# Performance work log

Hardware: AMD Instinct MI355X
Metric: run time of the kernel (lower is better)

## Reference

```python
import jax, jax.numpy as jnp
import numpy as np

EMBED_DIM = 1024
NUM_HEADS = 16
HEAD_DIM = EMBED_DIM // NUM_HEADS
BSZ = 4
SEQ = 1500


def setup_inputs() -> dict:
    key = jax.random.key(0)
    ks = jax.random.split(key, 8)
    s = 0.02
    return {
        "hidden_states": jax.random.normal(ks[0], (BSZ, SEQ, EMBED_DIM), jnp.float32),
        "Wq": jax.random.normal(ks[1], (EMBED_DIM, EMBED_DIM), jnp.float32) * s,
        "bq": jax.random.normal(ks[2], (EMBED_DIM,), jnp.float32) * s,
        "Wk": jax.random.normal(ks[3], (EMBED_DIM, EMBED_DIM), jnp.float32) * s,
        "Wv": jax.random.normal(ks[4], (EMBED_DIM, EMBED_DIM), jnp.float32) * s,
        "bv": jax.random.normal(ks[5], (EMBED_DIM,), jnp.float32) * s,
        "Wo": jax.random.normal(ks[6], (EMBED_DIM, EMBED_DIM), jnp.float32) * s,
        "bo": jax.random.normal(ks[7], (EMBED_DIM,), jnp.float32) * s,
    }


def reference(hidden_states, Wq, bq, Wk, Wv, bv, Wo, bo):
    b, t, e = hidden_states.shape
    h, d = NUM_HEADS, HEAD_DIM
    scaling = d ** -0.5

    def shape(x):  # [b, t, e] -> [b, h, t, d]
        return x.reshape(b, t, h, d).transpose(0, 2, 1, 3)

    # q_proj (with bias) then scale applied to the full projected output,
    # matching the original (scale multiplies q_proj output incl. bias).
    q = shape((hidden_states @ Wq.T + bq) * scaling)
    k = shape(hidden_states @ Wk.T)            # k_proj has no bias in Whisper
    v = shape(hidden_states @ Wv.T + bv)

    # naive materialized attention scores: [b, h, t, t]
    attn_weights = jnp.einsum("bhqd,bhkd->bhqk", q, k)
    attn_probs = jax.nn.softmax(attn_weights, axis=-1)
    attn_output = jnp.einsum("bhqk,bhkd->bhqd", attn_probs, v)

    # [b, h, t, d] -> [b, t, e]
    attn_output = attn_output.transpose(0, 2, 1, 3).reshape(b, t, e)
    return attn_output @ Wo.T + bo
```

## Files before the change

### kernel.cpp

```cpp
#include <hip/hip_runtime.h>
#include <math.h>

#define E 1024
#define NH 16
#define HD 64
#define BSZ_ 4
#define SEQ_ 1500
#define M_ (BSZ_ * SEQ_)
#define SZE ((size_t)M_ * (size_t)E)
#define QSC (0.125f * 1.44269504f)

#define QA_OFF  0u
#define XB_OFF  6144000u
#define WB_OFF  12288000u
#define WOB_OFF 15433728u
#define WS_NEED_BYTES ((size_t)(16482304u) * 2u)

typedef __attribute__((ext_vector_type(8))) short short8v;
typedef __attribute__((ext_vector_type(4))) float f32x4;
typedef __attribute__((ext_vector_type(16))) float f32x16;
typedef __attribute__((ext_vector_type(4))) unsigned short ushort4v;

__device__ __forceinline__ unsigned short f2bf(float f) {
    union { float f; unsigned int i; } c; c.f = f;
    return (unsigned short)((c.i + 0x7FFFu + ((c.i >> 16) & 1u)) >> 16);
}
__device__ __forceinline__ unsigned int cvt_pk_bf16(float a, float b) {
    unsigned int r;
    asm("v_cvt_pk_bf16_f32 %0, %1, %2" : "=v"(r) : "v"(a), "v"(b));
    return r;
}
__device__ __forceinline__ void perml32(unsigned int &a, unsigned int &b) {
    asm("v_permlane32_swap_b32 %0, %1" : "+v"(a), "+v"(b));
}

__device__ __forceinline__ int swz(int row, int col) {
    return (row << 6) + ((((col >> 3) ^ row) & 7) << 3) + (col & 7);
}
__device__ __forceinline__ int swzf(int r, int d) {
    int row = r >> 1;
    int cs = ((r & 1) << 3) | (d >> 3);
    return row * 128 + ((cs ^ (row & 15)) << 3) + (d & 7);
}

__device__ __forceinline__ short8v pack8(const float* x) {
    union { unsigned int u[4]; short8v v; } r;
    r.u[0] = cvt_pk_bf16(x[0], x[1]);
    r.u[1] = cvt_pk_bf16(x[2], x[3]);
    r.u[2] = cvt_pk_bf16(x[4], x[5]);
    r.u[3] = cvt_pk_bf16(x[6], x[7]);
    return r.v;
}

__device__ __forceinline__ void gload16(const unsigned short* g,
                                        unsigned short* l) {
    __builtin_amdgcn_global_load_lds(
        (const __attribute__((address_space(1))) unsigned int*)(g),
        (__attribute__((address_space(3))) unsigned int*)(l), 16, 0, 0);
}


__global__ __launch_bounds__(256) void cvt_kernel(
    const float* __restrict__ X,  const float* __restrict__ Wk,
    const float* __restrict__ Wv, const float* __restrict__ Wq,
    const float* __restrict__ Wo, unsigned short* __restrict__ ws)
{
    size_t w = ((size_t)blockIdx.x * 256 + threadIdx.x) * 8;
    const float* s; unsigned short* d; float sc = 1.0f;
    if (w < 6144000u)      { s = X  + w;             d = ws + XB_OFF + w; }
    else if (w < 7192576u) { s = Wk + (w - 6144000u); d = ws + WB_OFF + (w - 6144000u); }
    else if (w < 8241152u) { s = Wv + (w - 7192576u); d = ws + WB_OFF + 1048576u + (w - 7192576u); }
    else if (w < 9289728u) { s = Wq + (w - 8241152u); d = ws + WB_OFF + 2097152u + (w - 8241152u); sc = QSC; }
    else                   { s = Wo + (w - 9289728u); d = ws + WOB_OFF + (w - 9289728u); }
    float t[8];
    *(float4*)t = *(const float4*)s;
    *(float4*)(t + 4) = *(const float4*)(s + 4);
#pragma unroll
    for (int i = 0; i < 8; ++i) t[i] *= sc;
    *(short8v*)d = pack8(t);
}

__device__ __forceinline__ void gemm128b(
    const unsigned short* __restrict__ Arow,
    const unsigned short* __restrict__ Brow,
    unsigned short* As, unsigned short* Bs, int tid, f32x4 acc[4][4])
{
    const int lane = tid & 63, wid = tid >> 6;
    const int wm = tid >> 7, wn = (tid >> 6) & 1;
    for (int k0 = 0; k0 < E; k0 += 64) {
#pragma unroll
        for (int i = 0; i < 4; ++i) {
            int row = wid * 32 + i * 8 + (lane >> 3);
            int sl = (lane & 7) ^ (row & 7);
            unsigned short* lbase = As + (wid * 32 + i * 8) * 64;
            gload16(Arow + (size_t)row * E + k0 + sl * 8, lbase);
            unsigned short* lbase2 = Bs + (wid * 32 + i * 8) * 64;
            gload16(Brow + (size_t)row * E + k0 + sl * 8, lbase2);
        }
        __syncthreads();
#pragma unroll
        for (int kk = 0; kk < 64; kk += 32) {
            short8v afr[4], bfr[4];
#pragma unroll
            for (int m = 0; m < 4; ++m)
                afr[m] = *(const short8v*)(As + swz(wm * 64 + m * 16 + (lane & 15),
                                                    kk + (lane >> 4) * 8));
#pragma unroll
            for (int n = 0; n < 4; ++n)
                bfr[n] = *(const short8v*)(Bs + swz(wn * 64 + n * 16 + (lane & 15),
                                                    kk + (lane >> 4) * 8));
            __builtin_amdgcn_s_setprio(1);
#pragma unroll
            for (int m = 0; m < 4; ++m)
#pragma unroll
                for (int n = 0; n < 4; ++n)
                    acc[m][n] = __builtin_amdgcn_mfma_f32_16x16x32_bf16(
                        afr[m], bfr[n], acc[m][n], 0, 0, 0);
            __builtin_amdgcn_s_setprio(0);
        }
        __syncthreads();
    }
}

__global__ __launch_bounds__(256) void proj_fast(
    const unsigned short* __restrict__ Xb, const unsigned short* __restrict__ Wb,
    const float* __restrict__ bv, const float* __restrict__ bq,
    unsigned short* __restrict__ Kb, unsigned short* __restrict__ Vt,
    unsigned short* __restrict__ Qa)
{
    __shared__ unsigned short As[128 * 64], Bs[128 * 64];
    const int sid = blockIdx.x;
    const int nid = (sid & 7) * 141 + (sid >> 3);
    const int mb = nid / 24, nb = nid % 24;
    const int z = nb >> 3;
    const size_t m0 = (size_t)mb * 128;
    const int tid = threadIdx.x, lane = tid & 63;
    const int wm = tid >> 7, wn = (tid >> 6) & 1;

    f32x4 acc[4][4];
#pragma unroll
    for (int m = 0; m < 4; ++m)
#pragma unroll
        for (int n = 0; n < 4; ++n)
#pragma unroll
            for (int i = 0; i < 4; ++i) acc[m][n][i] = 0.f;

    gemm128b(Xb + m0 * E, Wb + (size_t)nb * 128 * E, As, Bs, tid, acc);

#pragma unroll
    for (int m = 0; m < 4; ++m) {
        long gi0 = (long)m0 + wm * 64 + m * 16 + (lane >> 4) * 4;
#pragma unroll
        for (int n = 0; n < 4; ++n) {
            int col = (nb & 7) * 128 + wn * 64 + n * 16 + (lane & 15);
            if (z == 0) {
#pragma unroll
                for (int rg = 0; rg < 4; ++rg) {
                    long gi = gi0 + rg;
                    if (gi < M_) Kb[(size_t)gi * E + col] = f2bf(acc[m][n][rg]);
                }
            } else if (z == 2) {
                float bias = bq[col] * QSC;
#pragma unroll
                for (int rg = 0; rg < 4; ++rg) {
                    long gi = gi0 + rg;
                    if (gi < M_)
                        Qa[(size_t)gi * E + col] = f2bf(acc[m][n][rg] + bias);
                }
            } else {
                float bias = bv[col];
                if (gi0 + 3 < M_) {
                    long bb = gi0 / SEQ_, t0 = gi0 % SEQ_;
                    union { unsigned int u[2]; ushort4v v; } pk;
                    pk.u[0] = cvt_pk_bf16(acc[m][n][0] + bias, acc[m][n][1] + bias);
                    pk.u[1] = cvt_pk_bf16(acc[m][n][2] + bias, acc[m][n][3] + bias);
                    *(ushort4v*)(Vt + ((size_t)bb * E + col) * SEQ_ + t0) = pk.v;
                } else {
#pragma unroll
                    for (int rg = 0; rg < 4; ++rg) {
                        long gi = gi0 + rg;
                        if (gi < M_) {
                            long bb = gi / SEQ_, t = gi % SEQ_;
                            Vt[((size_t)bb * E + col) * SEQ_ + t] =
                                f2bf(acc[m][n][rg] + bias);
                        }
                    }
                }
            }
        }
    }
}

__global__ __launch_bounds__(256) void oproj_fast(
    const unsigned short* __restrict__ Ab, const unsigned short* __restrict__ Wob,
    const float* __restrict__ bo, float* __restrict__ out)
{
    __shared__ unsigned short As[128 * 64], Bs[128 * 64];
    const int sid = blockIdx.x;
    const int nid = (sid & 7) * 47 + (sid >> 3);
    const int mb = nid >> 3, nb = nid & 7;
    const size_t m0 = (size_t)mb * 128;
    const int tid = threadIdx.x, lane = tid & 63;
    const int wm = tid >> 7, wn = (tid >> 6) & 1;

    f32x4 acc[4][4];
#pragma unroll
    for (int m = 0; m < 4; ++m)
#pragma unroll
        for (int n = 0; n < 4; ++n)
#pragma unroll
            for (int i = 0; i < 4; ++i) acc[m][n][i] = 0.f;

    gemm128b(Ab + m0 * E, Wob + (size_t)nb * 128 * E, As, Bs, tid, acc);

#pragma unroll
    for (int m = 0; m < 4; ++m) {
        long gi0 = (long)m0 + wm * 64 + m * 16 + (lane >> 4) * 4;
#pragma unroll
        for (int n = 0; n < 4; ++n) {
            int col = nb * 128 + wn * 64 + n * 16 + (lane & 15);
            float bias = bo[col];
#pragma unroll
            for (int rg = 0; rg < 4; ++rg) {
                long gi = gi0 + rg;
                if (gi < M_) out[(size_t)gi * E + col] = acc[m][n][rg] + bias;
            }
        }
    }
}

template <bool ABF>
__device__ __forceinline__ void gemm128(
    const float* __restrict__ Af, const unsigned short* __restrict__ Ab,
    size_t arow0, int avalid,
    const float* __restrict__ W, int wrow0,
    unsigned short* As, unsigned short* Bs,
    int tid, f32x4 acc[4][4])
{
    const int lane = tid & 63;
    const int wm = (tid >> 7), wn = (tid >> 6) & 1;
    float4 pA[8]; short8v pAb[4]; float4 pB[8];

    auto loadT = [&](int k0) {
#pragma unroll
        for (int uu = 0; uu < 4; ++uu) {
            int u = tid + uu * 256, row = u >> 3, sl = (u & 7) * 8;
            if constexpr (ABF) {
                short8v t;
#pragma unroll
                for (int i = 0; i < 8; ++i) t[i] = 0;
                if (row < avalid)
                    t = *(const short8v*)(Ab + (arow0 + row) * E + k0 + sl);
                pAb[uu] = t;
            } else {
                float4 x0 = make_float4(0.f, 0.f, 0.f, 0.f), x1 = x0;
                if (row < avalid) {
                    const float* p = Af + (arow0 + row) * (size_t)E + k0 + sl;
                    x0 = *(const float4*)p; x1 = *(const float4*)(p + 4);
                }
                pA[2 * uu] = x0; pA[2 * uu + 1] = x1;
            }
            const float* q = W + (size_t)(wrow0 + row) * E + k0 + sl;
            pB[2 * uu] = *(const float4*)q;
            pB[2 * uu + 1] = *(const float4*)(q + 4);
        }
    };
    auto commitT = [&]() {
#pragma unroll
        for (int uu = 0; uu < 4; ++uu) {
            int u = tid + uu * 256, row = u >> 3, sl = (u & 7) * 8;
            if constexpr (ABF) {
                *(short8v*)(As + swz(row, sl)) = pAb[uu];
            } else {
                float t[8];
                *(float4*)t = pA[2 * uu]; *(float4*)(t + 4) = pA[2 * uu + 1];
                *(short8v*)(As + swz(row, sl)) = pack8(t);
            }
            float t2[8];
            *(float4*)t2 = pB[2 * uu]; *(float4*)(t2 + 4) = pB[2 * uu + 1];
            *(short8v*)(Bs + swz(row, sl)) = pack8(t2);
        }
    };

    loadT(0);
    for (int k0 = 0; k0 < E; k0 += 64) {
        __syncthreads();
        commitT();
        __syncthreads();
        if (k0 + 64 < E) loadT(k0 + 64);
#pragma unroll
        for (int kk = 0; kk < 64; kk += 32) {
            short8v afr[4], bfr[4];
#pragma unroll
            for (int m = 0; m < 4; ++m)
                afr[m] = *(const short8v*)(As + swz(wm * 64 + m * 16 + (lane & 15),
                                                    kk + (lane >> 4) * 8));
#pragma unroll
            for (int n = 0; n < 4; ++n)
                bfr[n] = *(const short8v*)(Bs + swz(wn * 64 + n * 16 + (lane & 15),
                                                    kk + (lane >> 4) * 8));
            __builtin_amdgcn_s_setprio(1);
#pragma unroll
            for (int m = 0; m < 4; ++m)
#pragma unroll
                for (int n = 0; n < 4; ++n)
                    acc[m][n] = __builtin_amdgcn_mfma_f32_16x16x32_bf16(
                        afr[m], bfr[n], acc[m][n], 0, 0, 0);
            __builtin_amdgcn_s_setprio(0);
        }
    }
}

__global__ __launch_bounds__(256, 2) void proj_kernel(
    const float* __restrict__ X, const float* __restrict__ Wk,
    const float* __restrict__ Wv, const float* __restrict__ bv,
    const float* __restrict__ Wq, const float* __restrict__ bq,
    unsigned short* __restrict__ Kb, unsigned short* __restrict__ Vt,
    unsigned short* __restrict__ Qo)
{
    __shared__ unsigned short As[128 * 64], Bs[128 * 64];
    const int sid = blockIdx.x, cpx = gridDim.x >> 3;
    const int nid = (sid & 7) * cpx + (sid >> 3);
    const int mb = nid / 24, nb = nid % 24;
    const int z = nb >> 3, nbz = nb & 7;
    const size_t m0 = (size_t)mb * 128;
    const int avalid = (M_ - (int)m0) < 128 ? (M_ - (int)m0) : 128;
    const float* W = (z == 0) ? Wk : (z == 1) ? Wv : Wq;

    f32x4 acc[4][4];
#pragma unroll
    for (int m = 0; m < 4; ++m)
#pragma unroll
        for (int n = 0; n < 4; ++n)
#pragma unroll
            for (int i = 0; i < 4; ++i) acc[m][n][i] = 0.f;

    gemm128<false>(X, nullptr, m0, avalid, W, nbz * 128, As, Bs, threadIdx.x, acc);

    const int tid = threadIdx.x, lane = tid & 63;
    const int wm = (tid >> 7), wn = (tid >> 6) & 1;
#pragma unroll
    for (int m = 0; m < 4; ++m) {
        long gi0 = (long)m0 + wm * 64 + m * 16 + (lane >> 4) * 4;
#pragma unroll
        for (int n = 0; n < 4; ++n) {
            int col = nbz * 128 + wn * 64 + n * 16 + (lane & 15);
            if (z == 0) {
#pragma unroll
                for (int rg = 0; rg < 4; ++rg) {
                    long gi = gi0 + rg;
                    if (gi < M_) Kb[(size_t)gi * E + col] = f2bf(acc[m][n][rg]);
                }
            } else if (z == 2) {
                float bias = bq[col];
#pragma unroll
                for (int rg = 0; rg < 4; ++rg) {
                    long gi = gi0 + rg;
                    if (gi < M_)
                        Qo[(size_t)gi * E + col] = f2bf((acc[m][n][rg] + bias) * QSC);
                }
            } else {
                float bias = bv[col];
                if (gi0 + 3 < M_) {
                    long bb = gi0 / SEQ_, t0 = gi0 % SEQ_;
                    union { unsigned int u[2]; ushort4v v; } pk;
                    pk.u[0] = cvt_pk_bf16(acc[m][n][0] + bias, acc[m][n][1] + bias);
                    pk.u[1] = cvt_pk_bf16(acc[m][n][2] + bias, acc[m][n][3] + bias);
                    *(ushort4v*)(Vt + ((size_t)bb * E + col) * SEQ_ + t0) = pk.v;
                } else {
#pragma unroll
                    for (int rg = 0; rg < 4; ++rg) {
                        long gi = gi0 + rg;
                        if (gi < M_) {
                            long bb = gi / SEQ_, t = gi % SEQ_;
                            Vt[((size_t)bb * E + col) * SEQ_ + t] =
                                f2bf(acc[m][n][rg] + bias);
                        }
                    }
                }
            }
        }
    }
}

__global__ __launch_bounds__(256, 2) void oproj_kernel(
    const unsigned short* __restrict__ Ab, const float* __restrict__ Wo,
    const float* __restrict__ bo, float* __restrict__ out)
{
    __shared__ unsigned short As[128 * 64], Bs[128 * 64];
    const int sid = blockIdx.x, cpx = gridDim.x >> 3;
    const int nid = (sid & 7) * cpx + (sid >> 3);
    const int mb = nid >> 3, nb = nid & 7;
    const size_t m0 = (size_t)mb * 128;
    const int avalid = (M_ - (int)m0) < 128 ? (M_ - (int)m0) : 128;

    f32x4 acc[4][4];
#pragma unroll
    for (int m = 0; m < 4; ++m)
#pragma unroll
        for (int n = 0; n < 4; ++n)
#pragma unroll
            for (int i = 0; i < 4; ++i) acc[m][n][i] = 0.f;

    gemm128<true>(nullptr, Ab, m0, avalid, Wo, nb * 128, As, Bs, threadIdx.x, acc);

    const int tid = threadIdx.x, lane = tid & 63;
    const int wm = (tid >> 7), wn = (tid >> 6) & 1;
#pragma unroll
    for (int m = 0; m < 4; ++m) {
        long gi0 = (long)m0 + wm * 64 + m * 16 + (lane >> 4) * 4;
#pragma unroll
        for (int n = 0; n < 4; ++n) {
            int col = nb * 128 + wn * 64 + n * 16 + (lane & 15);
            float bias = bo[col];
#pragma unroll
            for (int rg = 0; rg < 4; ++rg) {
                long gi = gi0 + rg;
                if (gi < M_) out[(size_t)gi * E + col] = acc[m][n][rg] + bias;
            }
        }
    }
}

__global__ __launch_bounds__(256, 4) void attn_kernel(
    const unsigned short* __restrict__ Kb,
    const unsigned short* __restrict__ Vt,
    unsigned short* __restrict__ Qa)
{
    __shared__ unsigned short ks[2][32 * 128], vs[2][32 * 128];
    const int sid = blockIdx.x;
    const int nid = (sid & 7) * 96 + (sid >> 3);
    const int bh = nid / 12, qb = nid % 12;
    const int b = bh >> 4, hh = bh & 15;
    const int tid = threadIdx.x, lane = tid & 63, wz = tid >> 6;
    const int c = lane & 31, g2 = lane >> 5;
    const int q0 = qb * 128 + wz * 32;

    const unsigned short* kbase = Kb + (size_t)b * SEQ_ * E + hh * 64;
    const unsigned short* vbase = Vt + ((size_t)b * E + hh * 64) * SEQ_;

    short8v kreg[2];
    ushort4v vreg[4];
    auto loadK = [&](int kt0) {
#pragma unroll
        for (int uu = 0; uu < 2; ++uu) {
            int u = tid + uu * 256, key = u >> 3, slot = (u & 7) * 8;
            short8v t;
#pragma unroll
            for (int i = 0; i < 8; ++i) t[i] = 0;
            int gk = kt0 + key;
            if (gk < SEQ_) t = *(const short8v*)(kbase + (size_t)gk * E + slot);
            kreg[uu] = t;
        }
    };
    auto loadV = [&](int kt0) {
#pragma unroll
        for (int uu = 0; uu < 4; ++uu) {
            int u = tid + uu * 256, d = u >> 4, q4 = (u & 15) * 4;
            ushort4v t; t[0] = t[1] = t[2] = t[3] = 0;
            int col = kt0 + q4, rem = SEQ_ - col;
            const unsigned short* src = vbase + (size_t)d * SEQ_ + col;
            if (rem >= 4) t = *(const ushort4v*)src;
            else { for (int e2 = 0; e2 < 4; ++e2) if (e2 < rem) t[e2] = src[e2]; }
            vreg[uu] = t;
        }
    };
    auto commitKV = [&](unsigned short* kd, unsigned short* vd) {
#pragma unroll
        for (int uu = 0; uu < 2; ++uu) {
            int u = tid + uu * 256;
            *(short8v*)(kd + swzf(u >> 3, (u & 7) * 8)) = kreg[uu];
        }
#pragma unroll
        for (int uu = 0; uu < 4; ++uu) {
            int u = tid + uu * 256;
            *(ushort4v*)(vd + swzf(u >> 4, (u & 15) * 4)) = vreg[uu];
        }
    };

    loadK(0); loadV(0);

    short8v qf[4];
    {
        int qr = q0 + c;
        bool ok = qr < SEQ_;
        const unsigned short* qp = Qa + ((size_t)b * SEQ_ + qr) * E + hh * 64 + 8 * g2;
#pragma unroll
        for (int t = 0; t < 4; ++t) {
            short8v zv;
#pragma unroll
            for (int i = 0; i < 8; ++i) zv[i] = 0;
            if (ok) zv = *(const short8v*)(qp + t * 16);
            qf[t] = zv;
        }
    }

    f32x16 o0, o1;
#pragma unroll
    for (int i = 0; i < 16; ++i) { o0[i] = 0.f; o1[i] = 0.f; }
    float lsum = 0.f;

    commitKV(ks[0], vs[0]);
    __syncthreads();
    loadK(64); loadV(64);

    const int NT = (SEQ_ + 63) / 64;
    for (int it = 0; it < NT; ++it) {
        const int kt0 = it * 64;
        const unsigned short* kcur = ks[it & 1];
        const unsigned short* vcur = vs[it & 1];
        const bool tail = (kt0 + 64 > SEQ_);

#pragma unroll
        for (int nt = 0; nt < 2; ++nt) {
            f32x16 s;
#pragma unroll
            for (int i = 0; i < 16; ++i) s[i] = 0.f;
            __builtin_amdgcn_s_setprio(1);
#pragma unroll
            for (int t = 0; t < 4; ++t) {
                short8v af = *(const short8v*)(kcur + swzf(nt * 32 + c, t * 16 + 8 * g2));
                s = __builtin_amdgcn_mfma_f32_32x32x16_bf16(af, qf[t], s, 0, 0, 0);
            }
            __builtin_amdgcn_s_setprio(0);
            if (tail) {
#pragma unroll
                for (int r = 0; r < 16; ++r) {
                    int key = kt0 + nt * 32 + (r & 3) + 8 * (r >> 2) + 4 * g2;
                    if (key >= SEQ_) s[r] = -1e30f;
                }
            }
            unsigned int pk[8];
            float ls0 = 0.f, ls1 = 0.f;
#pragma unroll
            for (int h = 0; h < 8; ++h) {
                float p0 = __builtin_amdgcn_exp2f(s[2 * h]);
                float p1 = __builtin_amdgcn_exp2f(s[2 * h + 1]);
                if (h & 1) ls1 += p0 + p1; else ls0 += p0 + p1;
                pk[h] = cvt_pk_bf16(p0, p1);
            }
            lsum += ls0 + ls1;
            perml32(pk[0], pk[2]); perml32(pk[1], pk[3]);
            perml32(pk[4], pk[6]); perml32(pk[5], pk[7]);
            __builtin_amdgcn_s_setprio(1);
#pragma unroll
            for (int tau = 0; tau < 2; ++tau) {
                union { unsigned int w[4]; short8v v; } pa;
                pa.w[0] = pk[4 * tau + 0];
                pa.w[1] = pk[4 * tau + 1];
                pa.w[2] = pk[4 * tau + 2];
                pa.w[3] = pk[4 * tau + 3];
                int t = nt * 2 + tau;
                short8v vb0 = *(const short8v*)(vcur + swzf(0 + c, t * 16 + 8 * g2));
                short8v vb1 = *(const short8v*)(vcur + swzf(32 + c, t * 16 + 8 * g2));
                o0 = __builtin_amdgcn_mfma_f32_32x32x16_bf16(pa.v, vb0, o0, 0, 0, 0);
                o1 = __builtin_amdgcn_mfma_f32_32x32x16_bf16(pa.v, vb1, o1, 0, 0, 0);
            }
            __builtin_amdgcn_s_setprio(0);
        }

        if (it + 1 < NT) {
            commitKV(ks[(it + 1) & 1], vs[(it + 1) & 1]);
            __syncthreads();
            if (it + 2 < NT) { loadK(kt0 + 128); loadV(kt0 + 128); }
        }
    }

    lsum += __shfl_xor(lsum, 32, 64);
    __syncthreads();
    float* lf = (float*)ks[0] + wz * 32;
    if (lane < 32) lf[c] = 1.0f / lsum;
#pragma unroll
    for (int r = 0; r < 16; ++r) {
        int ql = (r & 3) + 8 * (r >> 2) + 4 * g2;
        int tq = q0 + ql;
        if (tq < SEQ_) {
            float inv = lf[ql];
            unsigned short* op = Qa + ((size_t)b * SEQ_ + tq) * E + hh * 64;
            op[c] = f2bf(o0[r] * inv);
            op[32 + c] = f2bf(o1[r] * inv);
        }
    }
}

extern "C" void kernel_launch(void* const* d_in, const int* in_sizes, int n_in,
                              void* d_out, int out_size, void* d_ws, size_t ws_size,
                              hipStream_t stream) {
    const float* hs = (const float*)d_in[0];
    const float* Wq = (const float*)d_in[1];
    const float* bq = (const float*)d_in[2];
    const float* Wk = (const float*)d_in[3];
    const float* Wv = (const float*)d_in[4];
    const float* bv = (const float*)d_in[5];
    const float* Wo = (const float*)d_in[6];
    const float* bo = (const float*)d_in[7];

    unsigned short* Kb = (unsigned short*)d_out;
    unsigned short* Vt = (unsigned short*)d_out + SZE;
    unsigned short* ws = (unsigned short*)d_ws;
    unsigned short* Qa = ws + QA_OFF;
    float* out = (float*)d_out;

    if (ws_size >= WS_NEED_BYTES) {
        cvt_kernel<<<dim3(5048), 256, 0, stream>>>(hs, Wk, Wv, Wq, Wo, ws);
        proj_fast<<<dim3(1128), 256, 0, stream>>>(ws + XB_OFF, ws + WB_OFF,
                                                  bv, bq, Kb, Vt, Qa);
        attn_kernel<<<dim3(768), 256, 0, stream>>>(Kb, Vt, Qa);
        oproj_fast<<<dim3(376), 256, 0, stream>>>(Qa, ws + WOB_OFF, bo, out);
    } else {
        proj_kernel<<<dim3(47 * 24), 256, 0, stream>>>(hs, Wk, Wv, bv, Wq, bq,
                                                       Kb, Vt, Qa);
        attn_kernel<<<dim3(768), 256, 0, stream>>>(Kb, Vt, Qa);
        oproj_kernel<<<dim3(47 * 8), 256, 0, stream>>>(Qa, Wo, bo, out);
    }
}
```

Before: 182.3 us.

## Split attention over key halves with partial outputs and a combine kernel

```diff
diff --git a/kernel.cpp b/kernel.cpp
--- a/kernel.cpp
+++ b/kernel.cpp
@@ -15,6 +15,8 @@
 #define WB_OFF  12288000u
 #define WOB_OFF 15433728u
 #define WS_NEED_BYTES ((size_t)(16482304u) * 2u)
+#define PART_BYTE_OFF 32964608u
+#define WS3_NEED_BYTES (82884608ull)
 
 typedef __attribute__((ext_vector_type(8))) short short8v;
 typedef __attribute__((ext_vector_type(4))) float f32x4;
@@ -58,7 +60,6 @@
         (const __attribute__((address_space(1))) unsigned int*)(g),
         (__attribute__((address_space(3))) unsigned int*)(l), 16, 0, 0);
 }
-
 
 __global__ __launch_bounds__(256) void cvt_kernel(
     const float* __restrict__ X,  const float* __restrict__ Wk,
@@ -422,6 +423,184 @@
     }
 }
 
+__global__ __launch_bounds__(256, 4) void attn_ks(
+    const unsigned short* __restrict__ Kb,
+    const unsigned short* __restrict__ Vt,
+    const unsigned short* __restrict__ Qa,
+    float* __restrict__ Pp, float* __restrict__ Lp)
+{
+    __shared__ unsigned short ks[32 * 128], vs[32 * 128];
+    const int sid = blockIdx.x;
+    const int nid = (sid & 7) * 192 + (sid >> 3);
+    const int bh = nid / 24, rest = nid % 24;
+    const int qb = rest >> 1, kh = rest & 1;
+    const int b = bh >> 4, hh = bh & 15;
+    const int tid = threadIdx.x, lane = tid & 63, wz = tid >> 6;
+    const int c = lane & 31, g2 = lane >> 5;
+    const int q0 = qb * 128 + wz * 32;
+
+    const unsigned short* kbase = Kb + (size_t)b * SEQ_ * E + hh * 64;
+    const unsigned short* vbase = Vt + ((size_t)b * E + hh * 64) * SEQ_;
+    float* Po = Pp + (size_t)kh * SZE;
+    float* Lo = Lp + (size_t)kh * (64 * SEQ_);
+
+    short8v kreg[2];
+    ushort4v vreg[4];
+    auto loadK = [&](int kt0) {
+#pragma unroll
+        for (int uu = 0; uu < 2; ++uu) {
+            int u = tid + uu * 256, key = u >> 3, slot = (u & 7) * 8;
+            short8v t;
+#pragma unroll
+            for (int i = 0; i < 8; ++i) t[i] = 0;
+            int gk = kt0 + key;
+            if (gk < SEQ_) t = *(const short8v*)(kbase + (size_t)gk * E + slot);
+            kreg[uu] = t;
+        }
+    };
+    auto loadV = [&](int kt0) {
+#pragma unroll
+        for (int uu = 0; uu < 4; ++uu) {
+            int u = tid + uu * 256, d = u >> 4, q4 = (u & 15) * 4;
+            ushort4v t; t[0] = t[1] = t[2] = t[3] = 0;
+            int col = kt0 + q4, rem = SEQ_ - col;
+            const unsigned short* src = vbase + (size_t)d * SEQ_ + col;
+            if (rem >= 4) t = *(const ushort4v*)src;
+            else { for (int e2 = 0; e2 < 4; ++e2) if (e2 < rem) t[e2] = src[e2]; }
+            vreg[uu] = t;
+        }
+    };
+    auto commitKV = [&]() {
+#pragma unroll
+        for (int uu = 0; uu < 2; ++uu) {
+            int u = tid + uu * 256;
+            *(short8v*)(ks + swzf(u >> 3, (u & 7) * 8)) = kreg[uu];
+        }
+#pragma unroll
+        for (int uu = 0; uu < 4; ++uu) {
+            int u = tid + uu * 256;
+            *(ushort4v*)(vs + swzf(u >> 4, (u & 15) * 4)) = vreg[uu];
+        }
+    };
+
+    const int tbeg = kh * 12, tend = tbeg + 12;
+    loadK(tbeg * 64); loadV(tbeg * 64);
+
+    short8v qf[4];
+    {
+        int qr = q0 + c;
+        bool ok = qr < SEQ_;
+        const unsigned short* qp = Qa + ((size_t)b * SEQ_ + qr) * E + hh * 64 + 8 * g2;
+#pragma unroll
+        for (int t = 0; t < 4; ++t) {
+            short8v zv;
+#pragma unroll
+            for (int i = 0; i < 8; ++i) zv[i] = 0;
+            if (ok) zv = *(const short8v*)(qp + t * 16);
+            qf[t] = zv;
+        }
+    }
+
+    f32x16 o0, o1;
+#pragma unroll
+    for (int i = 0; i < 16; ++i) { o0[i] = 0.f; o1[i] = 0.f; }
+    float lsum = 0.f;
+
+    for (int it = tbeg; it < tend; ++it) {
+        const int kt0 = it * 64;
+        __syncthreads();
+        commitKV();
+        __syncthreads();
+        if (it + 1 < tend) { loadK(kt0 + 64); loadV(kt0 + 64); }
+        const bool tail = (kt0 + 64 > SEQ_);
+
+#pragma unroll
+        for (int nt = 0; nt < 2; ++nt) {
+            f32x16 s;
+#pragma unroll
+            for (int i = 0; i < 16; ++i) s[i] = 0.f;
+            __builtin_amdgcn_s_setprio(1);
+#pragma unroll
+            for (int t = 0; t < 4; ++t) {
+                short8v af = *(const short8v*)(ks + swzf(nt * 32 + c, t * 16 + 8 * g2));
+                s = __builtin_amdgcn_mfma_f32_32x32x16_bf16(af, qf[t], s, 0, 0, 0);
+            }
+            __builtin_amdgcn_s_setprio(0);
+            if (tail) {
+#pragma unroll
+                for (int r = 0; r < 16; ++r) {
+                    int key = kt0 + nt * 32 + (r & 3) + 8 * (r >> 2) + 4 * g2;
+                    if (key >= SEQ_) s[r] = -1e30f;
+                }
+            }
+            unsigned int pk[8];
+            float ls0 = 0.f, ls1 = 0.f;
+#pragma unroll
+            for (int h = 0; h < 8; ++h) {
+                float p0 = __builtin_amdgcn_exp2f(s[2 * h]);
+                float p1 = __builtin_amdgcn_exp2f(s[2 * h + 1]);
+                if (h & 1) ls1 += p0 + p1; else ls0 += p0 + p1;
+                pk[h] = cvt_pk_bf16(p0, p1);
+            }
+            lsum += ls0 + ls1;
+            perml32(pk[0], pk[2]); perml32(pk[1], pk[3]);
+            perml32(pk[4], pk[6]); perml32(pk[5], pk[7]);
+            __builtin_amdgcn_s_setprio(1);
+#pragma unroll
+            for (int tau = 0; tau < 2; ++tau) {
+                union { unsigned int w[4]; short8v v; } pa;
+                pa.w[0] = pk[4 * tau + 0];
+                pa.w[1] = pk[4 * tau + 1];
+                pa.w[2] = pk[4 * tau + 2];
+                pa.w[3] = pk[4 * tau + 3];
+                int t = nt * 2 + tau;
+                short8v vb0 = *(const short8v*)(vs + swzf(0 + c, t * 16 + 8 * g2));
+                short8v vb1 = *(const short8v*)(vs + swzf(32 + c, t * 16 + 8 * g2));
+                o0 = __builtin_amdgcn_mfma_f32_32x32x16_bf16(pa.v, vb0, o0, 0, 0, 0);
+                o1 = __builtin_amdgcn_mfma_f32_32x32x16_bf16(pa.v, vb1, o1, 0, 0, 0);
+            }
+            __builtin_amdgcn_s_setprio(0);
+        }
+    }
+
+    lsum += __shfl_xor(lsum, 32, 64);
+    if (lane < 32) {
+        int tq = q0 + c;
+        if (tq < SEQ_) Lo[(size_t)bh * SEQ_ + tq] = lsum;
+    }
+#pragma unroll
+    for (int r = 0; r < 16; ++r) {
+        int ql = (r & 3) + 8 * (r >> 2) + 4 * g2;
+        int tq = q0 + ql;
+        if (tq < SEQ_) {
+            float* op = Po + ((size_t)b * SEQ_ + tq) * E + hh * 64;
+            op[c] = o0[r];
+            op[32 + c] = o1[r];
+        }
+    }
+}
+
+__global__ __launch_bounds__(256) void combine_kernel(
+    const float* __restrict__ Pp, const float* __restrict__ Lp,
+    unsigned short* __restrict__ Qa)
+{
+    size_t i8 = ((size_t)blockIdx.x * 256 + threadIdx.x) * 8;
+    size_t row = i8 >> 10;
+    int e = (int)(i8 & 1023);
+    int bh = (int)(row / SEQ_) * 16 + (e >> 6);
+    int t = (int)(row % SEQ_);
+    size_t li = (size_t)bh * SEQ_ + t;
+    float inv = 1.0f / (Lp[li] + Lp[(size_t)64 * SEQ_ + li]);
+    const float* p0 = Pp + i8;
+    const float* p1 = Pp + SZE + i8;
+    float t0[8], t1[8], r8[8];
+    *(float4*)t0 = *(const float4*)p0; *(float4*)(t0 + 4) = *(const float4*)(p0 + 4);
+    *(float4*)t1 = *(const float4*)p1; *(float4*)(t1 + 4) = *(const float4*)(p1 + 4);
+#pragma unroll
+    for (int i = 0; i < 8; ++i) r8[i] = (t0[i] + t1[i]) * inv;
+    *(short8v*)(Qa + i8) = pack8(r8);
+}
+
 __global__ __launch_bounds__(256, 4) void attn_kernel(
     const unsigned short* __restrict__ Kb,
     const unsigned short* __restrict__ Vt,
@@ -601,7 +780,16 @@
     unsigned short* Qa = ws + QA_OFF;
     float* out = (float*)d_out;
 
-    if (ws_size >= WS_NEED_BYTES) {
+    if (ws_size >= WS3_NEED_BYTES) {
+        float* Pf = (float*)((char*)d_ws + PART_BYTE_OFF);
+        float* Lf = Pf + 2 * SZE;
+        cvt_kernel<<<dim3(5048), 256, 0, stream>>>(hs, Wk, Wv, Wq, Wo, ws);
+        proj_fast<<<dim3(1128), 256, 0, stream>>>(ws + XB_OFF, ws + WB_OFF,
+                                                  bv, bq, Kb, Vt, Qa);
+        attn_ks<<<dim3(1536), 256, 0, stream>>>(Kb, Vt, Qa, Pf, Lf);
+        combine_kernel<<<dim3(3000), 256, 0, stream>>>(Pf, Lf, Qa);
+        oproj_fast<<<dim3(376), 256, 0, stream>>>(Qa, ws + WOB_OFF, bo, out);
+    } else if (ws_size >= WS_NEED_BYTES) {
         cvt_kernel<<<dim3(5048), 256, 0, stream>>>(hs, Wk, Wv, Wq, Wo, ws);
         proj_fast<<<dim3(1128), 256, 0, stream>>>(ws + XB_OFF, ws + WB_OFF,
                                                   bv, bq, Kb, Vt, Qa);
```

Measured after the change: 315.1 us. +72.9%, slower.

## Split attention key range across two warp groups per block and merge partial outputs

Applied to the files above, without the earlier changes.

```diff
diff --git a/kernel.cpp b/kernel.cpp
--- a/kernel.cpp
+++ b/kernel.cpp
@@ -58,7 +58,6 @@
         (const __attribute__((address_space(1))) unsigned int*)(g),
         (__attribute__((address_space(3))) unsigned int*)(l), 16, 0, 0);
 }
-
 
 __global__ __launch_bounds__(256) void cvt_kernel(
     const float* __restrict__ X,  const float* __restrict__ Wk,
@@ -422,19 +421,26 @@
     }
 }
 
-__global__ __launch_bounds__(256, 4) void attn_kernel(
+__global__ __launch_bounds__(512, 4) void attn_kernel2(
     const unsigned short* __restrict__ Kb,
     const unsigned short* __restrict__ Vt,
     unsigned short* __restrict__ Qa)
 {
-    __shared__ unsigned short ks[2][32 * 128], vs[2][32 * 128];
+    __shared__ unsigned short tiles[16384];
+    __shared__ float lsumb[128];
     const int sid = blockIdx.x;
     const int nid = (sid & 7) * 96 + (sid >> 3);
     const int bh = nid / 12, qb = nid % 12;
     const int b = bh >> 4, hh = bh & 15;
-    const int tid = threadIdx.x, lane = tid & 63, wz = tid >> 6;
+    const int tid = threadIdx.x;
+    const int kh = tid >> 8;
+    const int gtid = tid & 255;
+    const int lane = tid & 63, wz = (tid >> 6) & 3;
     const int c = lane & 31, g2 = lane >> 5;
     const int q0 = qb * 128 + wz * 32;
+
+    unsigned short* ks = tiles + kh * 4096;
+    unsigned short* vs = tiles + 8192 + kh * 4096;
 
     const unsigned short* kbase = Kb + (size_t)b * SEQ_ * E + hh * 64;
     const unsigned short* vbase = Vt + ((size_t)b * E + hh * 64) * SEQ_;
@@ -444,7 +450,7 @@
     auto loadK = [&](int kt0) {
 #pragma unroll
         for (int uu = 0; uu < 2; ++uu) {
-            int u = tid + uu * 256, key = u >> 3, slot = (u & 7) * 8;
+            int u = gtid + uu * 256, key = u >> 3, slot = (u & 7) * 8;
             short8v t;
 #pragma unroll
             for (int i = 0; i < 8; ++i) t[i] = 0;
@@ -456,29 +462,30 @@
     auto loadV = [&](int kt0) {
 #pragma unroll
         for (int uu = 0; uu < 4; ++uu) {
-            int u = tid + uu * 256, d = u >> 4, q4 = (u & 15) * 4;
+            int u = gtid + uu * 256, d = u >> 4, q4 = (u & 15) * 4;
             ushort4v t; t[0] = t[1] = t[2] = t[3] = 0;
             int col = kt0 + q4, rem = SEQ_ - col;
             const unsigned short* src = vbase + (size_t)d * SEQ_ + col;
             if (rem >= 4) t = *(const ushort4v*)src;
-            else { for (int e2 = 0; e2 < 4; ++e2) if (e2 < rem) t[e2] = src[e2]; }
+            else if (rem > 0) { for (int e2 = 0; e2 < 4; ++e2) if (e2 < rem) t[e2] = src[e2]; }
             vreg[uu] = t;
         }
     };
-    auto commitKV = [&](unsigned short* kd, unsigned short* vd) {
+    auto commitKV = [&]() {
 #pragma unroll
         for (int uu = 0; uu < 2; ++uu) {
-            int u = tid + uu * 256;
-            *(short8v*)(kd + swzf(u >> 3, (u & 7) * 8)) = kreg[uu];
+            int u = gtid + uu * 256;
+            *(short8v*)(ks + swzf(u >> 3, (u & 7) * 8)) = kreg[uu];
         }
 #pragma unroll
         for (int uu = 0; uu < 4; ++uu) {
-            int u = tid + uu * 256;
-            *(ushort4v*)(vd + swzf(u >> 4, (u & 15) * 4)) = vreg[uu];
+            int u = gtid + uu * 256;
+            *(ushort4v*)(vs + swzf(u >> 4, (u & 15) * 4)) = vreg[uu];
         }
     };
 
-    loadK(0); loadV(0);
+    const int kbeg = kh * 768;
+    loadK(kbeg); loadV(kbeg);
 
     short8v qf[4];
     {
@@ -500,15 +507,12 @@
     for (int i = 0; i < 16; ++i) { o0[i] = 0.f; o1[i] = 0.f; }
     float lsum = 0.f;
 
-    commitKV(ks[0], vs[0]);
-    __syncthreads();
-    loadK(64); loadV(64);
-
-    const int NT = (SEQ_ + 63) / 64;
-    for (int it = 0; it < NT; ++it) {
-        const int kt0 = it * 64;
-        const unsigned short* kcur = ks[it & 1];
-        const unsigned short* vcur = vs[it & 1];
+    for (int it = 0; it < 12; ++it) {
+        const int kt0 = kbeg + it * 64;
+        __syncthreads();
+        commitKV();
+        __syncthreads();
+        if (it + 1 < 12) { loadK(kt0 + 64); loadV(kt0 + 64); }
         const bool tail = (kt0 + 64 > SEQ_);
 
 #pragma unroll
@@ -519,7 +523,7 @@
             __builtin_amdgcn_s_setprio(1);
 #pragma unroll
             for (int t = 0; t < 4; ++t) {
-                short8v af = *(const short8v*)(kcur + swzf(nt * 32 + c, t * 16 + 8 * g2));
+                short8v af = *(const short8v*)(ks + swzf(nt * 32 + c, t * 16 + 8 * g2));
                 s = __builtin_amdgcn_mfma_f32_32x32x16_bf16(af, qf[t], s, 0, 0, 0);
             }
             __builtin_amdgcn_s_setprio(0);
@@ -551,34 +555,42 @@
                 pa.w[2] = pk[4 * tau + 2];
                 pa.w[3] = pk[4 * tau + 3];
                 int t = nt * 2 + tau;
-                short8v vb0 = *(const short8v*)(vcur + swzf(0 + c, t * 16 + 8 * g2));
-                short8v vb1 = *(const short8v*)(vcur + swzf(32 + c, t * 16 + 8 * g2));
+                short8v vb0 = *(const short8v*)(vs + swzf(0 + c, t * 16 + 8 * g2));
+                short8v vb1 = *(const short8v*)(vs + swzf(32 + c, t * 16 + 8 * g2));
                 o0 = __builtin_amdgcn_mfma_f32_32x32x16_bf16(pa.v, vb0, o0, 0, 0, 0);
                 o1 = __builtin_amdgcn_mfma_f32_32x32x16_bf16(pa.v, vb1, o1, 0, 0, 0);
             }
             __builtin_amdgcn_s_setprio(0);
         }
-
-        if (it + 1 < NT) {
-            commitKV(ks[(it + 1) & 1], vs[(it + 1) & 1]);
-            __syncthreads();
-            if (it + 2 < NT) { loadK(kt0 + 128); loadV(kt0 + 128); }
-        }
     }
 
     lsum += __shfl_xor(lsum, 32, 64);
     __syncthreads();
-    float* lf = (float*)ks[0] + wz * 32;
-    if (lane < 32) lf[c] = 1.0f / lsum;
-#pragma unroll
-    for (int r = 0; r < 16; ++r) {
-        int ql = (r & 3) + 8 * (r >> 2) + 4 * g2;
-        int tq = q0 + ql;
-        if (tq < SEQ_) {
-            float inv = lf[ql];
-            unsigned short* op = Qa + ((size_t)b * SEQ_ + tq) * E + hh * 64;
-            op[c] = f2bf(o0[r] * inv);
-            op[32 + c] = f2bf(o1[r] * inv);
+    float* comb = (float*)tiles;
+    float* cw = comb + wz * 2048;
+    if (kh == 1) {
+#pragma unroll
+        for (int r = 0; r < 16; ++r) {
+            int ql = (r & 3) + 8 * (r >> 2) + 4 * g2;
+            cw[ql * 64 + c] = o0[r];
+            cw[ql * 64 + 32 + c] = o1[r];
+        }
+        if (lane < 32) lsumb[wz * 32 + c] = lsum;
+    }
+    __syncthreads();
+    if (kh == 0) {
+        float* lf = lsumb + wz * 32;
+        if (lane < 32) lf[c] = 1.0f / (lsum + lf[c]);
+#pragma unroll
+        for (int r = 0; r < 16; ++r) {
+            int ql = (r & 3) + 8 * (r >> 2) + 4 * g2;
+            int tq = q0 + ql;
+            if (tq < SEQ_) {
+                float inv = lf[ql];
+                unsigned short* op = Qa + ((size_t)b * SEQ_ + tq) * E + hh * 64;
+                op[c] = f2bf((o0[r] + cw[ql * 64 + c]) * inv);
+                op[32 + c] = f2bf((o1[r] + cw[ql * 64 + 32 + c]) * inv);
+            }
         }
     }
 }
@@ -605,12 +617,12 @@
         cvt_kernel<<<dim3(5048), 256, 0, stream>>>(hs, Wk, Wv, Wq, Wo, ws);
         proj_fast<<<dim3(1128), 256, 0, stream>>>(ws + XB_OFF, ws + WB_OFF,
                                                   bv, bq, Kb, Vt, Qa);
-        attn_kernel<<<dim3(768), 256, 0, stream>>>(Kb, Vt, Qa);
+        attn_kernel2<<<dim3(768), 512, 0, stream>>>(Kb, Vt, Qa);
         oproj_fast<<<dim3(376), 256, 0, stream>>>(Qa, ws + WOB_OFF, bo, out);
     } else {
         proj_kernel<<<dim3(47 * 24), 256, 0, stream>>>(hs, Wk, Wv, bv, Wq, bq,
                                                        Kb, Vt, Qa);
-        attn_kernel<<<dim3(768), 256, 0, stream>>>(Kb, Vt, Qa);
+        attn_kernel2<<<dim3(768), 512, 0, stream>>>(Kb, Vt, Qa);
         oproj_kernel<<<dim3(47 * 8), 256, 0, stream>>>(Qa, Wo, bo, out);
     }
 }
```

After: 195.8 us. 7.4% more time.

## Add attention kernel staging K/V via direct global-to-LDS loads with padded V

Applied to the files above, without the earlier changes.

```diff
diff --git a/kernel.cpp b/kernel.cpp
--- a/kernel.cpp
+++ b/kernel.cpp
@@ -6,6 +6,7 @@
 #define HD 64
 #define BSZ_ 4
 #define SEQ_ 1500
+#define VSTR 1504
 #define M_ (BSZ_ * SEQ_)
 #define SZE ((size_t)M_ * (size_t)E)
 #define QSC (0.125f * 1.44269504f)
@@ -14,7 +15,10 @@
 #define XB_OFF  6144000u
 #define WB_OFF  12288000u
 #define WOB_OFF 15433728u
-#define WS_NEED_BYTES ((size_t)(16482304u) * 2u)
+#define VT_OFF  16482304u
+#define CVT_TOTAL 10338304u
+#define PAD_ELEMS 18432u
+#define WS_FAST_BYTES 45289472ull
 
 typedef __attribute__((ext_vector_type(8))) short short8v;
 typedef __attribute__((ext_vector_type(4))) float f32x4;
@@ -59,13 +63,27 @@
         (__attribute__((address_space(3))) unsigned int*)(l), 16, 0, 0);
 }
 
-
 __global__ __launch_bounds__(256) void cvt_kernel(
     const float* __restrict__ X,  const float* __restrict__ Wk,
     const float* __restrict__ Wv, const float* __restrict__ Wq,
     const float* __restrict__ Wo, unsigned short* __restrict__ ws)
 {
     size_t w = ((size_t)blockIdx.x * 256 + threadIdx.x) * 8;
+    if (w >= CVT_TOTAL) {
+        size_t p0 = w - CVT_TOTAL;
+        unsigned short* Vt = ws + VT_OFF;
+#pragma unroll
+        for (int i = 0; i < 8; ++i) {
+            size_t e = p0 + i;
+            if (e < 16384u) {
+                size_t row = e >> 2;
+                Vt[row * VSTR + 1500 + (e & 3)] = 0;
+            } else if (e < PAD_ELEMS) {
+                Vt[(size_t)4096 * VSTR + (e - 16384u)] = 0;
+            }
+        }
+        return;
+    }
     const float* s; unsigned short* d; float sc = 1.0f;
     if (w < 6144000u)      { s = X  + w;             d = ws + XB_OFF + w; }
     else if (w < 7192576u) { s = Wk + (w - 6144000u); d = ws + WB_OFF + (w - 6144000u); }
@@ -174,14 +192,14 @@
                     union { unsigned int u[2]; ushort4v v; } pk;
                     pk.u[0] = cvt_pk_bf16(acc[m][n][0] + bias, acc[m][n][1] + bias);
                     pk.u[1] = cvt_pk_bf16(acc[m][n][2] + bias, acc[m][n][3] + bias);
-                    *(ushort4v*)(Vt + ((size_t)bb * E + col) * SEQ_ + t0) = pk.v;
+                    *(ushort4v*)(Vt + ((size_t)bb * E + col) * VSTR + t0) = pk.v;
                 } else {
 #pragma unroll
                     for (int rg = 0; rg < 4; ++rg) {
                         long gi = gi0 + rg;
                         if (gi < M_) {
                             long bb = gi / SEQ_, t = gi % SEQ_;
-                            Vt[((size_t)bb * E + col) * SEQ_ + t] =
+                            Vt[((size_t)bb * E + col) * VSTR + t] =
                                 f2bf(acc[m][n][rg] + bias);
                         }
                     }
@@ -225,6 +243,132 @@
                 long gi = gi0 + rg;
                 if (gi < M_) out[(size_t)gi * E + col] = acc[m][n][rg] + bias;
             }
+        }
+    }
+}
+
+__global__ __launch_bounds__(256, 4) void attn_gl(
+    const unsigned short* __restrict__ Kb,
+    const unsigned short* __restrict__ Vt,
+    unsigned short* __restrict__ Qa)
+{
+    __shared__ unsigned short ks[4096], vs[4096];
+    const int sid = blockIdx.x;
+    const int nid = (sid & 7) * 96 + (sid >> 3);
+    const int bh = nid / 12, qb = nid % 12;
+    const int b = bh >> 4, hh = bh & 15;
+    const int tid = threadIdx.x, lane = tid & 63, wz = tid >> 6;
+    const int c = lane & 31, g2 = lane >> 5;
+    const int q0 = qb * 128 + wz * 32;
+
+    const unsigned short* kbase = Kb + (size_t)b * SEQ_ * E + hh * 64;
+    const unsigned short* vbase = Vt + ((size_t)b * E + hh * 64) * VSTR;
+
+    auto stageKV = [&](int kt0) {
+#pragma unroll
+        for (int i = 0; i < 2; ++i) {
+            int j = (i * 4 + wz) * 64 + lane;
+            int rp = j >> 4;
+            int u = (j & 15) ^ (rp & 15);
+            int r = rp * 2 + (u >> 3);
+            int s = u & 7;
+            gload16(kbase + (size_t)(kt0 + r) * E + s * 8,
+                    ks + (i * 4 + wz) * 512);
+            gload16(vbase + (size_t)r * VSTR + kt0 + s * 8,
+                    vs + (i * 4 + wz) * 512);
+        }
+    };
+
+    short8v qf[4];
+    {
+        int qr = q0 + c;
+        bool ok = qr < SEQ_;
+        const unsigned short* qp = Qa + ((size_t)b * SEQ_ + qr) * E + hh * 64 + 8 * g2;
+#pragma unroll
+        for (int t = 0; t < 4; ++t) {
+            short8v zv;
+#pragma unroll
+            for (int i = 0; i < 8; ++i) zv[i] = 0;
+            if (ok) zv = *(const short8v*)(qp + t * 16);
+            qf[t] = zv;
+        }
+    }
+
+    f32x16 o0, o1;
+#pragma unroll
+    for (int i = 0; i < 16; ++i) { o0[i] = 0.f; o1[i] = 0.f; }
+    float lsum = 0.f;
+
+    const int NT = (SEQ_ + 63) / 64;
+    for (int it = 0; it < NT; ++it) {
+        const int kt0 = it * 64;
+        __syncthreads();
+        stageKV(kt0);
+        __syncthreads();
+        const bool tail = (kt0 + 64 > SEQ_);
+
+#pragma unroll
+        for (int nt = 0; nt < 2; ++nt) {
+            f32x16 s;
+#pragma unroll
+            for (int i = 0; i < 16; ++i) s[i] = 0.f;
+            __builtin_amdgcn_s_setprio(1);
+#pragma unroll
+            for (int t = 0; t < 4; ++t) {
+                short8v af = *(const short8v*)(ks + swzf(nt * 32 + c, t * 16 + 8 * g2));
+                s = __builtin_amdgcn_mfma_f32_32x32x16_bf16(af, qf[t], s, 0, 0, 0);
+            }
+            __builtin_amdgcn_s_setprio(0);
+            if (tail) {
+#pragma unroll
+                for (int r = 0; r < 16; ++r) {
+                    int key = kt0 + nt * 32 + (r & 3) + 8 * (r >> 2) + 4 * g2;
+                    if (key >= SEQ_) s[r] = -1e30f;
+                }
+            }
+            unsigned int pk[8];
+            float ls0 = 0.f, ls1 = 0.f;
+#pragma unroll
+            for (int h = 0; h < 8; ++h) {
+                float p0 = __builtin_amdgcn_exp2f(s[2 * h]);
+                float p1 = __builtin_amdgcn_exp2f(s[2 * h + 1]);
+                if (h & 1) ls1 += p0 + p1; else ls0 += p0 + p1;
+                pk[h] = cvt_pk_bf16(p0, p1);
+            }
+            lsum += ls0 + ls1;
+            perml32(pk[0], pk[2]); perml32(pk[1], pk[3]);
+            perml32(pk[4], pk[6]); perml32(pk[5], pk[7]);
+            __builtin_amdgcn_s_setprio(1);
+#pragma unroll
+            for (int tau = 0; tau < 2; ++tau) {
+                union { unsigned int ww[4]; short8v v; } pa;
+                pa.ww[0] = pk[4 * tau + 0];
+                pa.ww[1] = pk[4 * tau + 1];
+                pa.ww[2] = pk[4 * tau + 2];
+                pa.ww[3] = pk[4 * tau + 3];
+                int t = nt * 2 + tau;
+                short8v vb0 = *(const short8v*)(vs + swzf(0 + c, t * 16 + 8 * g2));
+                short8v vb1 = *(const short8v*)(vs + swzf(32 + c, t * 16 + 8 * g2));
+                o0 = __builtin_amdgcn_mfma_f32_32x32x16_bf16(pa.v, vb0, o0, 0, 0, 0);
+                o1 = __builtin_amdgcn_mfma_f32_32x32x16_bf16(pa.v, vb1, o1, 0, 0, 0);
+            }
+            __builtin_amdgcn_s_setprio(0);
+        }
+    }
+
+    lsum += __shfl_xor(lsum, 32, 64);
+    __syncthreads();
+    float* lf = (float*)ks + wz * 32;
+    if (lane < 32) lf[c] = 1.0f / lsum;
+#pragma unroll
+    for (int r = 0; r < 16; ++r) {
+        int ql = (r & 3) + 8 * (r >> 2) + 4 * g2;
+        int tq = q0 + ql;
+        if (tq < SEQ_) {
+            float inv = lf[ql];
+            unsigned short* op = Qa + ((size_t)b * SEQ_ + tq) * E + hh * 64;
+            op[c] = f2bf(o0[r] * inv);
+            op[32 + c] = f2bf(o1[r] * inv);
         }
     }
 }
@@ -422,7 +566,7 @@
     }
 }
 
-__global__ __launch_bounds__(256, 4) void attn_kernel(
+__global__ __launch_bounds__(256, 4) void attn_fallback(
     const unsigned short* __restrict__ Kb,
     const unsigned short* __restrict__ Vt,
     unsigned short* __restrict__ Qa)
@@ -461,7 +605,7 @@
             int col = kt0 + q4, rem = SEQ_ - col;
             const unsigned short* src = vbase + (size_t)d * SEQ_ + col;
             if (rem >= 4) t = *(const ushort4v*)src;
-            else { for (int e2 = 0; e2 < 4; ++e2) if (e2 < rem) t[e2] = src[e2]; }
+            else if (rem > 0) { for (int e2 = 0; e2 < 4; ++e2) if (e2 < rem) t[e2] = src[e2]; }
             vreg[uu] = t;
         }
     };
@@ -516,13 +660,11 @@
             f32x16 s;
 #pragma unroll
             for (int i = 0; i < 16; ++i) s[i] = 0.f;
-            __builtin_amdgcn_s_setprio(1);
 #pragma unroll
             for (int t = 0; t < 4; ++t) {
                 short8v af = *(const short8v*)(kcur + swzf(nt * 32 + c, t * 16 + 8 * g2));
                 s = __builtin_amdgcn_mfma_f32_32x32x16_bf16(af, qf[t], s, 0, 0, 0);
             }
-            __builtin_amdgcn_s_setprio(0);
             if (tail) {
 #pragma unroll
                 for (int r = 0; r < 16; ++r) {
@@ -542,21 +684,19 @@
             lsum += ls0 + ls1;
             perml32(pk[0], pk[2]); perml32(pk[1], pk[3]);
             perml32(pk[4], pk[6]); perml32(pk[5], pk[7]);
-            __builtin_amdgcn_s_setprio(1);
 #pragma unroll
             for (int tau = 0; tau < 2; ++tau) {
-                union { unsigned int w[4]; short8v v; } pa;
-                pa.w[0] = pk[4 * tau + 0];
-                pa.w[1] = pk[4 * tau + 1];
-                pa.w[2] = pk[4 * tau + 2];
-                pa.w[3] = pk[4 * tau + 3];
+                union { unsigned int ww[4]; short8v v; } pa;
+                pa.ww[0] = pk[4 * tau + 0];
+                pa.ww[1] = pk[4 * tau + 1];
+                pa.ww[2] = pk[4 * tau + 2];
+                pa.ww[3] = pk[4 * tau + 3];
                 int t = nt * 2 + tau;
                 short8v vb0 = *(const short8v*)(vcur + swzf(0 + c, t * 16 + 8 * g2));
                 short8v vb1 = *(const short8v*)(vcur + swzf(32 + c, t * 16 + 8 * g2));
                 o0 = __builtin_amdgcn_mfma_f32_32x32x16_bf16(pa.v, vb0, o0, 0, 0, 0);
                 o1 = __builtin_amdgcn_mfma_f32_32x32x16_bf16(pa.v, vb1, o1, 0, 0, 0);
             }
-            __builtin_amdgcn_s_setprio(0);
         }
 
         if (it + 1 < NT) {
@@ -596,21 +736,22 @@
     const float* bo = (const float*)d_in[7];
 
     unsigned short* Kb = (unsigned short*)d_out;
-    unsigned short* Vt = (unsigned short*)d_out + SZE;
     unsigned short* ws = (unsigned short*)d_ws;
     unsigned short* Qa = ws + QA_OFF;
     float* out = (float*)d_out;
 
-    if (ws_size >= WS_NEED_BYTES) {
-        cvt_kernel<<<dim3(5048), 256, 0, stream>>>(hs, Wk, Wv, Wq, Wo, ws);
+    if (ws_size >= WS_FAST_BYTES) {
+        unsigned short* Vt = ws + VT_OFF;
+        cvt_kernel<<<dim3(5057), 256, 0, stream>>>(hs, Wk, Wv, Wq, Wo, ws);
         proj_fast<<<dim3(1128), 256, 0, stream>>>(ws + XB_OFF, ws + WB_OFF,
                                                   bv, bq, Kb, Vt, Qa);
-        attn_kernel<<<dim3(768), 256, 0, stream>>>(Kb, Vt, Qa);
+        attn_gl<<<dim3(768), 256, 0, stream>>>(Kb, Vt, Qa);
         oproj_fast<<<dim3(376), 256, 0, stream>>>(Qa, ws + WOB_OFF, bo, out);
     } else {
+        unsigned short* Vt = (unsigned short*)d_out + SZE;
         proj_kernel<<<dim3(47 * 24), 256, 0, stream>>>(hs, Wk, Wv, bv, Wq, bq,
                                                        Kb, Vt, Qa);
-        attn_kernel<<<dim3(768), 256, 0, stream>>>(Kb, Vt, Qa);
+        attn_fallback<<<dim3(768), 256, 0, stream>>>(Kb, Vt, Qa);
         oproj_kernel<<<dim3(47 * 8), 256, 0, stream>>>(Qa, Wo, bo, out);
     }
 }
```

New measurement: 160.4 us. 12.0% less time.
